# Kernel tuning notes

Hardware: AMD Instinct MI355X
Metric: run time of the kernel (lower is better)

## Reference

```python
import jax, jax.numpy as jnp
import numpy as np

FC = 16  # feat_channel
EPS = 1e-4


def _sch_forward(sch_feat, conv_weight, mask, target, pre_ind, ind):
    B, C, H, W = sch_feat.shape
    M = pre_ind.shape[1]
    fc = FC
    # _tranpose_and_gather_feat: gather per-object weight vectors at pre_ind
    cw = conv_weight.reshape(B, conv_weight.shape[1], H * W)          # B,Wt,HW
    weight = jnp.take_along_axis(cw, pre_ind[:, None, :], axis=2)    # B,Wt,M
    weight = jnp.transpose(weight, (0, 2, 1))                         # B,M,Wt
    # split into the 3-layer dynamic MLP params
    s1 = (fc + 2) * fc
    w1 = weight[..., :s1].reshape(B, M, fc, fc + 2)
    b1 = weight[..., s1:s1 + fc]
    s2 = s1 + fc
    w2 = weight[..., s2:s2 + fc * fc].reshape(B, M, fc, fc)
    b2 = weight[..., s2 + fc * fc:s2 + fc * fc + fc]
    s3 = s2 + fc * fc + fc
    w3 = weight[..., s3:s3 + fc]                                      # B,M,fc (1 out channel)
    b3 = weight[..., s3 + fc:s3 + fc + 1]                             # B,M,1
    # relative coordinate grids; note torch: x = pre_ind % w (int), y = pre_ind / w (true div)
    x = (pre_ind % W).astype(jnp.float32)
    y = pre_ind.astype(jnp.float32) / W
    xg = jnp.arange(W, dtype=jnp.float32)
    yg = jnp.arange(H, dtype=jnp.float32)
    x_rel = (xg[None, None, None, :] - x[:, :, None, None]) / 128.0   # B,M,1,W
    y_rel = (yg[None, None, :, None] - y[:, :, None, None]) / 128.0   # B,M,H,1
    x_rel = jnp.broadcast_to(x_rel, (B, M, H, W))
    y_rel = jnp.broadcast_to(y_rel, (B, M, H, W))
    feat = jnp.concatenate([
        jnp.broadcast_to(sch_feat[:, None], (B, M, C, H, W)),
        x_rel[:, :, None], y_rel[:, :, None]], axis=2)                # B,M,fc+2,H,W
    # three grouped 1x1 convs == per-instance matmuls
    h = jax.nn.relu(jnp.einsum('bmchw,bmoc->bmohw', feat, w1) + b1[:, :, :, None, None])
    h = jax.nn.relu(jnp.einsum('bmchw,bmoc->bmohw', h, w2) + b2[:, :, :, None, None])
    hm = jnp.einsum('bmchw,bmc->bmhw', h, w3) + b3[:, :, :, None]      # B,M,H,W
    hm = jnp.clip(jax.nn.sigmoid(hm), EPS, 1.0 - EPS)                  # _sigmoid
    # FastFocalLoss over (B*M, 1, H, W) with cat = 0
    neg_loss = jnp.sum(jnp.log(1.0 - hm) * hm ** 2 * (1.0 - target) ** 4)
    hm_flat = hm.reshape(B, M, H * W)
    pos_pred = jnp.take_along_axis(hm_flat, ind[..., None], axis=2)[..., 0]  # B,M
    pos_loss = jnp.sum(jnp.log(pos_pred) * (1.0 - pos_pred) ** 2 * mask)
    num_pos = jnp.sum(mask)
    loss = jnp.where(num_pos == 0,
                     -neg_loss,
                     -(pos_loss + neg_loss) / jnp.maximum(num_pos, 1.0))
    return loss


def setup_inputs() -> dict:
    key = jax.random.key(0)
    k1, k2, k3, k4, k5 = jax.random.split(key, 5)
    B, M, H, W = 4, 32, 152, 272
    Wt = (FC + 2) * FC + FC + FC * FC + FC + FC + 1  # 593
    return {
        'sch_feat': jax.random.normal(k1, (B, FC, H, W), dtype=jnp.float32),
        'conv_weight': jax.random.normal(k2, (B, Wt, H, W), dtype=jnp.float32),
        'mask': jnp.ones((B, M), dtype=jnp.float32),
        'pre_ind': jax.random.randint(k3, (B, M), 0, H * W, dtype=jnp.int64) if jax.config.jax_enable_x64 else jax.random.randint(k3, (B, M), 0, H * W).astype(jnp.int32),
        'target': jax.random.uniform(k4, (B, M, H, W), dtype=jnp.float32),
        'ind': jax.random.randint(k5, (B, M), 0, H * W).astype(jnp.int32),
    }


def reference(sch_feat, conv_weight, mask, pre_ind, target, ind):
    return _sch_forward(sch_feat, conv_weight, mask, target, pre_ind, ind)
```

## Files before the change

kernel.cpp:

```cpp
#include <hip/hip_runtime.h>

typedef unsigned int uint;
typedef unsigned short ushort;
typedef unsigned char uint8_t_;

constexpr int Bc = 4, Mc = 32, Hc = 152, Wc = 272;
constexpr int HWc = Hc * Wc;
constexpr int WTc = 593;
constexpr int NB = 8;
constexpr int NEG_BLOCKS = Bc * Mc * NB;
constexpr int ITERS = HWc / 64;
constexpr int POS_OFF = 1024;
constexpr int WC_OFF = 2048;
constexpr int WC_STRIDE = 600;
constexpr int APK1_OFF = WC_OFF + 128 * WC_STRIDE;
constexpr int APK2_OFF = APK1_OFF + 128 * 64 * 4;
constexpr size_t XOFF_BYTES = (size_t)(APK2_OFF + 128 * 64 * 4) * 4;
constexpr int GRPB = HWc / 16;
constexpr int GSTRIDE = 576;
constexpr int XCVT_BLOCKS = 162 * Bc;

using f32x4 = __attribute__((ext_vector_type(4))) float;
using bf16x8 = __attribute__((ext_vector_type(8))) short;

__device__ inline uint pkbf(float lo, float hi) {
  uint r;
  asm("v_cvt_pk_bf16_f32 %0, %1, %2" : "=v"(r) : "v"(lo), "v"(hi));
  return r;
}
__device__ inline float bpermf(int byteaddr, float v) {
  return __int_as_float(__builtin_amdgcn_ds_bpermute(byteaddr, __float_as_int(v)));
}
__device__ inline uint bpermu(int byteaddr, uint v) {
  return (uint)__builtin_amdgcn_ds_bpermute(byteaddr, (int)v);
}

union FR { uint u[4]; bf16x8 v; };

__global__ __launch_bounds__(256) void fused_pre(const float* __restrict__ sf_all,
                                                 const float* __restrict__ cw,
                                                 const int* __restrict__ pre_ind,
                                                 const int* __restrict__ ind,
                                                 const float* __restrict__ mask,
                                                 unsigned char* __restrict__ xb,
                                                 float* __restrict__ ws) {
  __shared__ float sw[WTc];
  const int blk = blockIdx.x, tid = threadIdx.x;

  if (blk < XCVT_BLOCKS) {
    const int b = blk / 162, bx = blk - b * 162;
    const int px = bx * 256 + tid;
    if (px < HWc) {
      const float* s = sf_all + (size_t)b * 16 * HWc + px;
      uint q[8];
#pragma unroll
      for (int i = 0; i < 8; i++) q[i] = pkbf(s[(size_t)(2 * i) * HWc], s[(size_t)(2 * i + 1) * HWc]);
      const int hh = px / Wc, xx = px - hh * Wc;
      const uint q8 = pkbf((float)xx * 0.0078125f, (float)hh * 0.0078125f);
      const int grp = px >> 4, o = px & 15;
      unsigned char* gb = xb + ((size_t)b * GRPB + grp) * GSTRIDE;
      *(uint4*)(gb + o * 16) = make_uint4(q[0], q[1], q[2], q[3]);
      *(uint4*)(gb + 256 + o * 16) = make_uint4(q[4], q[5], q[6], q[7]);
      *(uint*)(gb + 512 + o * 4) = q8;
    }
    return;
  }

  const int bm = blk - XCVT_BLOCKS, b = bm >> 5;
  const int p = pre_ind[bm];
  const float* wcol = cw + (size_t)b * WTc * HWc + p;
  float* wc = ws + WC_OFF + bm * WC_STRIDE;
  for (int j = tid; j < WTc; j += 256) {
    float v = wcol[(size_t)j * HWc];
    sw[j] = v;
    wc[j] = v;
  }
  __syncthreads();

  if (tid < 64) {
    const int g = tid >> 4, o = tid & 15;
    float a1f[8], a2f[8];
#pragma unroll
    for (int e = 0; e < 8; e++) {
      int k = 8 * g + e;
      a1f[e] = (k < 18) ? sw[o * 18 + k] : 0.0f;
      a2f[e] = (k < 16) ? sw[304 + o * 16 + k] : 0.0f;
    }
    uint4 u1, u2;
    u1.x = pkbf(a1f[0], a1f[1]); u1.y = pkbf(a1f[2], a1f[3]);
    u1.z = pkbf(a1f[4], a1f[5]); u1.w = pkbf(a1f[6], a1f[7]);
    u2.x = pkbf(a2f[0], a2f[1]); u2.y = pkbf(a2f[2], a2f[3]);
    u2.z = pkbf(a2f[4], a2f[5]); u2.w = pkbf(a2f[6], a2f[7]);
    ((uint4*)(ws + APK1_OFF))[bm * 64 + tid] = u1;
    ((uint4*)(ws + APK2_OFF))[bm * 64 + tid] = u2;
  } else if (tid == 64) {
    const float* sf = sf_all + (size_t)b * 16 * HWc;
    const int pi = ind[bm];
    float f[18];
#pragma unroll
    for (int c = 0; c < 16; c++) f[c] = sf[(size_t)c * HWc + pi];
    const int hh = pi / Wc;
    const float x0 = (float)(p % Wc);
    const float y0 = (float)p / (float)Wc;
    f[16] = ((float)(pi - hh * Wc) - x0) * 0.0078125f;
    f[17] = ((float)hh - y0) * 0.0078125f;
    float h1[16];
    for (int oo = 0; oo < 16; oo++) {
      float a = sw[288 + oo];
#pragma unroll
      for (int c = 0; c < 18; c++) a = fmaf(sw[oo * 18 + c], f[c], a);
      h1[oo] = fmaxf(a, 0.0f);
    }
    float h2[16];
    for (int oo = 0; oo < 16; oo++) {
      float a = sw[560 + oo];
#pragma unroll
      for (int c = 0; c < 16; c++) a = fmaf(sw[304 + oo * 16 + c], h1[c], a);
      h2[oo] = fmaxf(a, 0.0f);
    }
    float zv = sw[592];
#pragma unroll
    for (int c = 0; c < 16; c++) zv = fmaf(sw[576 + c], h2[c], zv);
    float hm = __fdividef(1.0f, 1.0f + __expf(-zv));
    hm = fminf(fmaxf(hm, 1e-4f), 1.0f - 1e-4f);
    const float om = 1.0f - hm;
    ws[POS_OFF + bm] = __logf(hm) * om * om * mask[bm];
  }
}

__global__ __launch_bounds__(256, 4) void sch_neg(const float* __restrict__ target,
                                                  const unsigned char* __restrict__ xbf,
                                                  const int* __restrict__ pre_ind,
                                                  float* __restrict__ ws) {
  const int tid = threadIdx.x;
  const int lane = tid & 63;
  const int wid = tid >> 6;
  const int xcd = blockIdx.x & 7;
  const int slot = blockIdx.x >> 3;
  const int b = xcd >> 1;
  const int m = slot & 31;
  const int nb = ((slot >> 5) << 1) | (xcd & 1);
  const int bm = (b << 5) | m;
  const int g = lane >> 4;
  const int o = lane & 15;

  const int p = pre_ind[bm];
  const float x0 = (float)(p % Wc);
  const float y0 = (float)p / (float)Wc;

  FR A1, A2;
  {
    uint4 u1 = ((const uint4*)(ws + APK1_OFF))[bm * 64 + lane];
    uint4 u2 = ((const uint4*)(ws + APK2_OFF))[bm * 64 + lane];
    A1.u[0] = u1.x; A1.u[1] = u1.y; A1.u[2] = u1.z; A1.u[3] = u1.w;
    A2.u[0] = u2.x; A2.u[1] = u2.y; A2.u[2] = u2.z; A2.u[3] = u2.w;
  }
  const float* wc = ws + WC_OFF + bm * WC_STRIDE;
  f32x4 c1v, c2v;
  float w3r[4];
#pragma unroll
  for (int r = 0; r < 4; r++) {
    int row = 4 * g + r;
    c1v[r] = wc[288 + row] - (wc[row * 18 + 16] * x0 + wc[row * 18 + 17] * y0) * 0.0078125f;
    c2v[r] = wc[560 + row];
    w3r[r] = wc[576 + row];
  }
  const float b3 = wc[592];

  const unsigned char* xb = xbf + (size_t)b * GRPB * GSTRIDE;
  const float* tg = target + (size_t)bm * HWc;

  const int aX16 = (lane ^ 16) << 2;
  const int aX32 = (lane ^ 32) << 2;
  const int aS0 = (o + ((g == 1) ? 32 : 0)) << 2;
  const int aS1 = (o + ((g == 1) ? 48 : 16)) << 2;
  const int offA = (g << 8) + (o << 4);
  const int offC = 512 + (o << 2);

  auto loadB1 = [&](int grpidx, uint4& q) {
    const unsigned char* gb = xb + (size_t)grpidx * GSTRIDE;
    if (g < 2) q = *(const uint4*)(gb + offA);
    else if (g == 2) q.x = *(const uint*)(gb + offC);
  };

  float acc = 0.0f;
  const int gw = nb * 4 + wid;

  uint4 ld[4];
  float tval;
#pragma unroll
  for (int c = 0; c < 4; c++) { ld[c] = make_uint4(0, 0, 0, 0); loadB1(gw * 4 + c, ld[c]); }
  tval = tg[gw * 64 + lane];

  for (int it = gw; it < ITERS; it += 32) {
    const int nit = (it + 32 < ITERS) ? it + 32 : it;
    uint4 ldn[4];
    float tvn;
#pragma unroll
    for (int c = 0; c < 4; c++) { ldn[c] = make_uint4(0, 0, 0, 0); loadB1(nit * 4 + c, ldn[c]); }
    tvn = tg[nit * 64 + lane];

    float zpv[4];
#pragma unroll
    for (int half = 0; half < 2; half++) {
      FR B1a, B1b;
      B1a.u[0] = ld[2 * half].x; B1a.u[1] = ld[2 * half].y;
      B1a.u[2] = ld[2 * half].z; B1a.u[3] = ld[2 * half].w;
      B1b.u[0] = ld[2 * half + 1].x; B1b.u[1] = ld[2 * half + 1].y;
      B1b.u[2] = ld[2 * half + 1].z; B1b.u[3] = ld[2 * half + 1].w;
      f32x4 d1a = __builtin_amdgcn_mfma_f32_16x16x32_bf16(A1.v, B1a.v, c1v, 0, 0, 0);
      f32x4 d1b = __builtin_amdgcn_mfma_f32_16x16x32_bf16(A1.v, B1b.v, c1v, 0, 0, 0);
      uint pa0 = pkbf(fmaxf(d1a[0], 0.0f), fmaxf(d1a[1], 0.0f));
      uint pa1 = pkbf(fmaxf(d1a[2], 0.0f), fmaxf(d1a[3], 0.0f));
      uint pb0 = pkbf(fmaxf(d1b[0], 0.0f), fmaxf(d1b[1], 0.0f));
      uint pb1 = pkbf(fmaxf(d1b[2], 0.0f), fmaxf(d1b[3], 0.0f));
      FR B2a, B2b;
      B2a.u[0] = bpermu(aS0, pa0); B2a.u[1] = bpermu(aS0, pa1);
      B2a.u[2] = bpermu(aS1, pa0); B2a.u[3] = bpermu(aS1, pa1);
      B2b.u[0] = bpermu(aS0, pb0); B2b.u[1] = bpermu(aS0, pb1);
      B2b.u[2] = bpermu(aS1, pb0); B2b.u[3] = bpermu(aS1, pb1);
      f32x4 d2a = __builtin_amdgcn_mfma_f32_16x16x32_bf16(A2.v, B2a.v, c2v, 0, 0, 0);
      f32x4 d2b = __builtin_amdgcn_mfma_f32_16x16x32_bf16(A2.v, B2b.v, c2v, 0, 0, 0);
      zpv[2 * half] = fmaxf(d2a[0], 0.0f) * w3r[0] + fmaxf(d2a[1], 0.0f) * w3r[1] +
                      fmaxf(d2a[2], 0.0f) * w3r[2] + fmaxf(d2a[3], 0.0f) * w3r[3];
      zpv[2 * half + 1] = fmaxf(d2b[0], 0.0f) * w3r[0] + fmaxf(d2b[1], 0.0f) * w3r[1] +
                          fmaxf(d2b[2], 0.0f) * w3r[2] + fmaxf(d2b[3], 0.0f) * w3r[3];
    }
    const int b0 = g & 1, b1 = g & 2;
    const float pk_g  = b1 ? (b0 ? zpv[3] : zpv[2]) : (b0 ? zpv[1] : zpv[0]);
    const float pk_g1 = b1 ? (b0 ? zpv[2] : zpv[3]) : (b0 ? zpv[0] : zpv[1]);
    const float pk_g2 = b1 ? (b0 ? zpv[1] : zpv[0]) : (b0 ? zpv[3] : zpv[2]);
    const float pk_g3 = b1 ? (b0 ? zpv[0] : zpv[1]) : (b0 ? zpv[2] : zpv[3]);
    const float tA = pk_g + bpermf(aX16, pk_g1);
    const float tB = pk_g2 + bpermf(aX16, pk_g3);
    const float S = tA + bpermf(aX32, tB);

    const float zz = S + b3;
    float hm = __fdividef(1.0f, 1.0f + __expf(-zz));
    hm = fminf(fmaxf(hm, 1e-4f), 1.0f - 1e-4f);
    const float u = 1.0f - tval;
    const float u2 = u * u;
    acc += __logf(1.0f - hm) * hm * hm * (u2 * u2);

#pragma unroll
    for (int c = 0; c < 4; c++) ld[c] = ldn[c];
    tval = tvn;
  }

  __shared__ float red[256];
  red[tid] = acc;
  __syncthreads();
  for (int s = 128; s > 0; s >>= 1) {
    if (tid < s) red[tid] += red[tid + s];
    __syncthreads();
  }
  if (tid == 0) ws[blockIdx.x] = red[0];
}

__global__ __launch_bounds__(256) void sch_final(const float* __restrict__ ws,
                                                 const float* __restrict__ mask,
                                                 float* __restrict__ out) {
  __shared__ float red[256];
  const int t = threadIdx.x;

  float s = 0.0f;
  for (int i = t; i < NEG_BLOCKS; i += 256) s += ws[i];
  red[t] = s; __syncthreads();
  for (int k = 128; k > 0; k >>= 1) { if (t < k) red[t] += red[t + k]; __syncthreads(); }
  const float neg = red[0];
  __syncthreads();

  float pv = (t < Bc * Mc) ? ws[POS_OFF + t] : 0.0f;
  red[t] = pv; __syncthreads();
  for (int k = 128; k > 0; k >>= 1) { if (t < k) red[t] += red[t + k]; __syncthreads(); }
  const float pos = red[0];
  __syncthreads();

  float mv = (t < Bc * Mc) ? mask[t] : 0.0f;
  red[t] = mv; __syncthreads();
  for (int k = 128; k > 0; k >>= 1) { if (t < k) red[t] += red[t + k]; __syncthreads(); }

  if (t == 0) {
    float np = red[0];
    out[0] = (np == 0.0f) ? (-neg) : (-(pos + neg) / fmaxf(np, 1.0f));
  }
}

extern "C" void kernel_launch(void* const* d_in, const int* in_sizes, int n_in,
                              void* d_out, int out_size, void* d_ws, size_t ws_size,
                              hipStream_t stream) {
  const float* sch_feat    = (const float*)d_in[0];
  const float* conv_weight = (const float*)d_in[1];
  const float* mask        = (const float*)d_in[2];
  const int*   pre_ind     = (const int*)d_in[3];
  const float* target      = (const float*)d_in[4];
  const int*   ind         = (const int*)d_in[5];
  float* out = (float*)d_out;
  float* ws  = (float*)d_ws;
  unsigned char* xbf = (unsigned char*)d_ws + XOFF_BYTES;

  fused_pre<<<dim3(XCVT_BLOCKS + Bc * Mc), dim3(256), 0, stream>>>(
      sch_feat, conv_weight, pre_ind, ind, mask, xbf, ws);
  sch_neg<<<dim3(NEG_BLOCKS), dim3(256), 0, stream>>>(target, xbf, pre_ind, ws);
  sch_final<<<dim3(1), dim3(256), 0, stream>>>(ws, mask, out);
}
```

Before: 51.35 us.

## Avoid layer-2 bpermute shuffles by re-packing A2 to match MFMA output layout

Layer-2 weights are now packed so each k-group holds only its own four output rows. The layer-1 MFMA output can then feed layer 2 directly, with the upper half of the B operand zeroed, which removes the ds_bpermute data shuffles. The final cross-lane sums switch to permlane16/32 swap builtins where available, falling back to shfl_xor. The explicit software prefetch of the next iteration's loads is dropped, and one MFMA pair per tile now does half-empty work.

```diff
diff --git a/kernel.cpp b/kernel.cpp
--- a/kernel.cpp
+++ b/kernel.cpp
@@ -2,7 +2,6 @@
 
 typedef unsigned int uint;
 typedef unsigned short ushort;
-typedef unsigned char uint8_t_;
 
 constexpr int Bc = 4, Mc = 32, Hc = 152, Wc = 272;
 constexpr int HWc = Hc * Wc;
@@ -28,11 +27,24 @@
   asm("v_cvt_pk_bf16_f32 %0, %1, %2" : "=v"(r) : "v"(lo), "v"(hi));
   return r;
 }
-__device__ inline float bpermf(int byteaddr, float v) {
-  return __int_as_float(__builtin_amdgcn_ds_bpermute(byteaddr, __float_as_int(v)));
-}
-__device__ inline uint bpermu(int byteaddr, uint v) {
-  return (uint)__builtin_amdgcn_ds_bpermute(byteaddr, (int)v);
+
+__device__ inline float xsum16(float x) {
+#if __has_builtin(__builtin_amdgcn_permlane16_swap)
+  uint u = __float_as_uint(x);
+  auto pr = __builtin_amdgcn_permlane16_swap(u, u, false, false);
+  return __uint_as_float(pr[0]) + __uint_as_float(pr[1]);
+#else
+  return x + __shfl_xor(x, 16);
+#endif
+}
+__device__ inline float xsum32(float x) {
+#if __has_builtin(__builtin_amdgcn_permlane32_swap)
+  uint u = __float_as_uint(x);
+  auto pr = __builtin_amdgcn_permlane32_swap(u, u, false, false);
+  return __uint_as_float(pr[0]) + __uint_as_float(pr[1]);
+#else
+  return x + __shfl_xor(x, 32);
+#endif
 }
 
 union FR { uint u[4]; bf16x8 v; };
@@ -84,7 +96,7 @@
     for (int e = 0; e < 8; e++) {
       int k = 8 * g + e;
       a1f[e] = (k < 18) ? sw[o * 18 + k] : 0.0f;
-      a2f[e] = (k < 16) ? sw[304 + o * 16 + k] : 0.0f;
+      a2f[e] = (e < 4) ? sw[304 + o * 16 + 4 * g + e] : 0.0f;
     }
     uint4 u1, u2;
     u1.x = pkbf(a1f[0], a1f[1]); u1.y = pkbf(a1f[2], a1f[3]);
@@ -170,81 +182,40 @@
   const unsigned char* xb = xbf + (size_t)b * GRPB * GSTRIDE;
   const float* tg = target + (size_t)bm * HWc;
 
-  const int aX16 = (lane ^ 16) << 2;
-  const int aX32 = (lane ^ 32) << 2;
-  const int aS0 = (o + ((g == 1) ? 32 : 0)) << 2;
-  const int aS1 = (o + ((g == 1) ? 48 : 16)) << 2;
-  const int offA = (g << 8) + (o << 4);
-  const int offC = 512 + (o << 2);
-
-  auto loadB1 = [&](int grpidx, uint4& q) {
-    const unsigned char* gb = xb + (size_t)grpidx * GSTRIDE;
-    if (g < 2) q = *(const uint4*)(gb + offA);
-    else if (g == 2) q.x = *(const uint*)(gb + offC);
-  };
+  const int addrOff = (g < 2) ? ((g << 8) + (o << 4)) : (512 + (o << 2));
 
   float acc = 0.0f;
   const int gw = nb * 4 + wid;
-
-  uint4 ld[4];
-  float tval;
-#pragma unroll
-  for (int c = 0; c < 4; c++) { ld[c] = make_uint4(0, 0, 0, 0); loadB1(gw * 4 + c, ld[c]); }
-  tval = tg[gw * 64 + lane];
-
   for (int it = gw; it < ITERS; it += 32) {
-    const int nit = (it + 32 < ITERS) ? it + 32 : it;
-    uint4 ldn[4];
-    float tvn;
-#pragma unroll
-    for (int c = 0; c < 4; c++) { ldn[c] = make_uint4(0, 0, 0, 0); loadB1(nit * 4 + c, ldn[c]); }
-    tvn = tg[nit * 64 + lane];
-
-    float zpv[4];
-#pragma unroll
-    for (int half = 0; half < 2; half++) {
-      FR B1a, B1b;
-      B1a.u[0] = ld[2 * half].x; B1a.u[1] = ld[2 * half].y;
-      B1a.u[2] = ld[2 * half].z; B1a.u[3] = ld[2 * half].w;
-      B1b.u[0] = ld[2 * half + 1].x; B1b.u[1] = ld[2 * half + 1].y;
-      B1b.u[2] = ld[2 * half + 1].z; B1b.u[3] = ld[2 * half + 1].w;
-      f32x4 d1a = __builtin_amdgcn_mfma_f32_16x16x32_bf16(A1.v, B1a.v, c1v, 0, 0, 0);
-      f32x4 d1b = __builtin_amdgcn_mfma_f32_16x16x32_bf16(A1.v, B1b.v, c1v, 0, 0, 0);
-      uint pa0 = pkbf(fmaxf(d1a[0], 0.0f), fmaxf(d1a[1], 0.0f));
-      uint pa1 = pkbf(fmaxf(d1a[2], 0.0f), fmaxf(d1a[3], 0.0f));
-      uint pb0 = pkbf(fmaxf(d1b[0], 0.0f), fmaxf(d1b[1], 0.0f));
-      uint pb1 = pkbf(fmaxf(d1b[2], 0.0f), fmaxf(d1b[3], 0.0f));
-      FR B2a, B2b;
-      B2a.u[0] = bpermu(aS0, pa0); B2a.u[1] = bpermu(aS0, pa1);
-      B2a.u[2] = bpermu(aS1, pa0); B2a.u[3] = bpermu(aS1, pa1);
-      B2b.u[0] = bpermu(aS0, pb0); B2b.u[1] = bpermu(aS0, pb1);
-      B2b.u[2] = bpermu(aS1, pb0); B2b.u[3] = bpermu(aS1, pb1);
-      f32x4 d2a = __builtin_amdgcn_mfma_f32_16x16x32_bf16(A2.v, B2a.v, c2v, 0, 0, 0);
-      f32x4 d2b = __builtin_amdgcn_mfma_f32_16x16x32_bf16(A2.v, B2b.v, c2v, 0, 0, 0);
-      zpv[2 * half] = fmaxf(d2a[0], 0.0f) * w3r[0] + fmaxf(d2a[1], 0.0f) * w3r[1] +
-                      fmaxf(d2a[2], 0.0f) * w3r[2] + fmaxf(d2a[3], 0.0f) * w3r[3];
-      zpv[2 * half + 1] = fmaxf(d2b[0], 0.0f) * w3r[0] + fmaxf(d2b[1], 0.0f) * w3r[1] +
-                          fmaxf(d2b[2], 0.0f) * w3r[2] + fmaxf(d2b[3], 0.0f) * w3r[3];
-    }
-    const int b0 = g & 1, b1 = g & 2;
-    const float pk_g  = b1 ? (b0 ? zpv[3] : zpv[2]) : (b0 ? zpv[1] : zpv[0]);
-    const float pk_g1 = b1 ? (b0 ? zpv[2] : zpv[3]) : (b0 ? zpv[0] : zpv[1]);
-    const float pk_g2 = b1 ? (b0 ? zpv[1] : zpv[0]) : (b0 ? zpv[3] : zpv[2]);
-    const float pk_g3 = b1 ? (b0 ? zpv[0] : zpv[1]) : (b0 ? zpv[2] : zpv[3]);
-    const float tA = pk_g + bpermf(aX16, pk_g1);
-    const float tB = pk_g2 + bpermf(aX16, pk_g3);
-    const float S = tA + bpermf(aX32, tB);
-
-    const float zz = S + b3;
+    const unsigned char* gb = xb + (size_t)(it * 4) * GSTRIDE;
+    uint4 ld[4];
+#pragma unroll
+    for (int c = 0; c < 4; c++) ld[c] = *(const uint4*)(gb + c * GSTRIDE + addrOff);
+    const float tval = tg[it * 64 + lane];
+
+    float Z[4];
+#pragma unroll
+    for (int c = 0; c < 4; c++) {
+      FR B1;
+      B1.u[0] = ld[c].x; B1.u[1] = ld[c].y; B1.u[2] = ld[c].z; B1.u[3] = ld[c].w;
+      f32x4 d1 = __builtin_amdgcn_mfma_f32_16x16x32_bf16(A1.v, B1.v, c1v, 0, 0, 0);
+      FR B2;
+      B2.u[0] = pkbf(fmaxf(d1[0], 0.0f), fmaxf(d1[1], 0.0f));
+      B2.u[1] = pkbf(fmaxf(d1[2], 0.0f), fmaxf(d1[3], 0.0f));
+      B2.u[2] = 0u;
+      B2.u[3] = 0u;
+      f32x4 d2 = __builtin_amdgcn_mfma_f32_16x16x32_bf16(A2.v, B2.v, c2v, 0, 0, 0);
+      float zp = fmaxf(d2[0], 0.0f) * w3r[0] + fmaxf(d2[1], 0.0f) * w3r[1] +
+                 fmaxf(d2[2], 0.0f) * w3r[2] + fmaxf(d2[3], 0.0f) * w3r[3];
+      Z[c] = xsum32(xsum16(zp));
+    }
+    float zz = (lane & 32) ? ((lane & 16) ? Z[3] : Z[2]) : ((lane & 16) ? Z[1] : Z[0]);
+    zz += b3;
     float hm = __fdividef(1.0f, 1.0f + __expf(-zz));
     hm = fminf(fmaxf(hm, 1e-4f), 1.0f - 1e-4f);
     const float u = 1.0f - tval;
     const float u2 = u * u;
     acc += __logf(1.0f - hm) * hm * hm * (u2 * u2);
-
-#pragma unroll
-    for (int c = 0; c < 4; c++) ld[c] = ldn[c];
-    tval = tvn;
   }
 
   __shared__ float red[256];
```

Result: faster. 50.08 us (-2.5%).
